# Kernel optimization log

Hardware: AMD Instinct MI355X
Metric: run time of the kernel (lower is better)

## Reference

```python
import jax, jax.numpy as jnp
import numpy as np

N_FEATURES = 170
D_MODEL = 64
N_HEADS = 4
ALPHA = 0.1
LN_EPS = 1e-5
LEAKY_SLOPE = 0.01  # torch F.leaky_relu default
N = 3 * N_FEATURES  # 510
B = 32


def setup_inputs() -> dict:
    key = jax.random.key(0)
    ks = jax.random.split(key, 10)
    D, H = D_MODEL, N_HEADS
    s = 1.0 / np.sqrt(D)
    return {
        "x": jax.random.normal(ks[0], (B, N, D), dtype=jnp.float32),
        "causal_graph": jax.random.uniform(ks[1], (N, N), dtype=jnp.float32),
        # nn.Linear(d_model, d_model*n_heads, bias=False): stored here as (D, H*D) for x @ W
        "W": jax.random.uniform(ks[2], (D, H * D), jnp.float32, -s, s),
        "attention_w": jax.random.normal(ks[3], (H, 2 * D), dtype=jnp.float32),
        # Conv2d(2, n_heads, 3, padding=1): OIHW kernel
        "conv_w": jax.random.uniform(ks[4], (H, 2, 3, 3), jnp.float32, -1/np.sqrt(18), 1/np.sqrt(18)),
        "conv_b": jax.random.uniform(ks[5], (H,), jnp.float32, -1/np.sqrt(18), 1/np.sqrt(18)),
        # nn.Linear(d_model, 2*d_model): stored as (D, 2D)
        "fcg_w": jax.random.uniform(ks[6], (D, 2 * D), jnp.float32, -s, s),
        "fcg_b": jax.random.uniform(ks[7], (2 * D,), jnp.float32, -s, s),
        "ln_g": jnp.ones((D,), jnp.float32),
        "ln_b": jnp.zeros((D,), jnp.float32),
    }


def reference(x, causal_graph, W, attention_w, conv_w, conv_b, fcg_w, fcg_b, ln_g, ln_b):
    Bz, Nn, D = x.shape
    H = N_HEADS
    # shared projection: (B, N, H, D)
    xt = (x @ W).reshape(Bz, Nn, H, D)
    # GAT-style additive scores: concat-dot decomposed into two dot products
    w1, w2 = attention_w[:, :D], attention_w[:, D:]  # each (H, D)
    s_i = jnp.einsum('bnhd,hd->bhn', xt, w1)  # source term
    s_j = jnp.einsum('bnhd,hd->bhn', xt, w2)  # target term
    e = s_i[:, :, :, None] + s_j[:, :, None, :]  # (B, H, N, N)
    A_eva = jnp.where(e >= 0, e, LEAKY_SLOPE * e)  # leaky_relu
    # fuse mean attention with causal graph via 3x3 conv
    A_mean = A_eva.mean(axis=1)  # (B, N, N)
    causal = jnp.broadcast_to(causal_graph[None], (Bz, Nn, Nn))
    stacked = jnp.stack([A_mean, causal], axis=1)  # (B, 2, N, N)
    A_st = jax.lax.conv_general_dilated(
        stacked, conv_w, window_strides=(1, 1), padding=((1, 1), (1, 1)),
        dimension_numbers=('NCHW', 'OIHW', 'NCHW'))
    A_st = A_st + conv_b[None, :, None, None]  # (B, H, N, N)
    A = jax.nn.softmax(ALPHA * A_eva + (1.0 - ALPHA) * A_st, axis=-1)
    # multi-head aggregation then head-mean
    out = jnp.einsum('bhnm,bmhd->bnhd', A, xt).mean(axis=2)  # (B, N, D)
    # GLU
    g = out @ fcg_w + fcg_b  # (B, N, 2D)
    a, b = g[..., :D], g[..., D:]
    glu = a * jax.nn.sigmoid(b)
    # residual + layernorm
    y = glu + x
    mu = y.mean(axis=-1, keepdims=True)
    var = ((y - mu) ** 2).mean(axis=-1, keepdims=True)
    y = (y - mu) * jax.lax.rsqrt(var + LN_EPS) * ln_g + ln_b
    return y, A
```

## Files before the change

### kernel.cpp

```cpp
#include <hip/hip_runtime.h>

#define Bz 32
#define Nn 510
#define Dd 64
#define Hh 4
#define HD_ 256
#define Kpad 512
#define ALPHA_ 0.1f
#define LNEPS 1e-5f
#define SLOPE 0.01f
#define NEG_INF -3.0e38f

typedef __attribute__((ext_vector_type(8))) short short8;
typedef __attribute__((ext_vector_type(4))) float floatx4;

__device__ inline float wredsum(float v) {
  #pragma unroll
  for (int off = 32; off; off >>= 1) v += __shfl_xor(v, off, 64);
  return v;
}
__device__ inline float wredmax(float v) {
  #pragma unroll
  for (int off = 32; off; off >>= 1) v = fmaxf(v, __shfl_xor(v, off, 64));
  return v;
}
__device__ inline unsigned short f2bf(float f) {
  unsigned int u = __float_as_uint(f);
  unsigned int r = (u + 0x7fffu + ((u >> 16) & 1u)) >> 16;
  return (unsigned short)r;
}

__global__ __launch_bounds__(256) void k1_xt(const float* __restrict__ x,
                                             const float* __restrict__ W,
                                             const float* __restrict__ attw,
                                             unsigned short* __restrict__ xtT,
                                             float* __restrict__ si,
                                             float* __restrict__ sj) {
  __shared__ float Wl[64][132];
  __shared__ float xr[32][68];
  const int t = threadIdx.x;
  const int rt = blockIdx.x;
  const int b = blockIdx.y;
  const int ch = blockIdx.z;
  #pragma unroll
  for (int k = 0; k < 8; k++) {
    int f = t + k * 256;
    int kr = f >> 5;
    int c = (f & 31) * 4;
    float4 v = *(const float4*)&W[kr * HD_ + ch * 128 + c];
    *(float4*)&Wl[kr][c] = v;
  }
  #pragma unroll
  for (int k = 0; k < 2; k++) {
    int f = t + k * 256;
    int r = f >> 4;
    int c = (f & 15) * 4;
    int row = rt * 32 + r;
    float4 v = make_float4(0.f, 0.f, 0.f, 0.f);
    if (row < Nn) v = *(const float4*)&x[(b * Nn + row) * Dd + c];
    *(float4*)&xr[r][c] = v;
  }
  __syncthreads();
  const int tr = t >> 5, tc = t & 31;
  const int rb = tr * 4, c0 = tc * 4;
  float acc[4][4] = {};
  #pragma unroll
  for (int k4 = 0; k4 < 16; k4++) {
    float4 xv[4];
    #pragma unroll
    for (int r = 0; r < 4; r++) xv[r] = *(float4*)&xr[rb + r][k4 * 4];
    #pragma unroll
    for (int kk = 0; kk < 4; kk++) {
      float4 wv = *(float4*)&Wl[k4 * 4 + kk][c0];
      #pragma unroll
      for (int r = 0; r < 4; r++) {
        float xs = (&xv[r].x)[kk];
        acc[r][0] = fmaf(xs, wv.x, acc[r][0]);
        acc[r][1] = fmaf(xs, wv.y, acc[r][1]);
        acc[r][2] = fmaf(xs, wv.z, acc[r][2]);
        acc[r][3] = fmaf(xs, wv.w, acc[r][3]);
      }
    }
  }
  const int colbase = ch * 128 + c0;
  const int h = colbase >> 6;
  const int dd = colbase & 63;
  const int m0r = rt * 32 + rb;
  #pragma unroll
  for (int cc = 0; cc < 4; cc++) {
    unsigned short* p = &xtT[((size_t)(b * 4 + h) * 64 + (dd + cc)) * Kpad + m0r];
    if (m0r + 3 < Nn) {
      ushort4 u;
      u.x = f2bf(acc[0][cc]); u.y = f2bf(acc[1][cc]);
      u.z = f2bf(acc[2][cc]); u.w = f2bf(acc[3][cc]);
      *(ushort4*)p = u;
    } else {
      #pragma unroll
      for (int r = 0; r < 4; r++) if (m0r + r < Nn) p[r] = f2bf(acc[r][cc]);
    }
  }
  float w1v[4], w2v[4];
  #pragma unroll
  for (int cc = 0; cc < 4; cc++) {
    w1v[cc] = attw[h * 128 + dd + cc];
    w2v[cc] = attw[h * 128 + 64 + dd + cc];
  }
  #pragma unroll
  for (int r = 0; r < 4; r++) {
    float p1 = acc[r][0] * w1v[0] + acc[r][1] * w1v[1] +
               acc[r][2] * w1v[2] + acc[r][3] * w1v[3];
    float p2 = acc[r][0] * w2v[0] + acc[r][1] * w2v[1] +
               acc[r][2] * w2v[2] + acc[r][3] * w2v[3];
    #pragma unroll
    for (int off = 1; off <= 8; off <<= 1) {
      p1 += __shfl_xor(p1, off, 64);
      p2 += __shfl_xor(p2, off, 64);
    }
    if ((tc & 15) == 0) {
      int row = m0r + r;
      if (row < Nn) {
        si[(b * 4 + h) * Nn + row] = p1;
        sj[(b * 4 + h) * Nn + row] = p2;
      }
    }
  }
}

__global__ __launch_bounds__(256) void k2_attn(const float* __restrict__ si,
                                               const float* __restrict__ sj,
                                               const float* __restrict__ causal,
                                               const float* __restrict__ convw,
                                               const float* __restrict__ convb,
                                               float* __restrict__ A) {
  __shared__ float am_t[10 * 8 * 68];
  __shared__ float cz_t[10 * 8 * 68];
  __shared__ float sjl[4 * 8 * 68];
  __shared__ float sil[4][12];
  const int t = threadIdx.x;
  const int i0 = blockIdx.x * 8;
  const int b = blockIdx.y;
  if (t < 40) {
    int h = t / 10, r = t % 10;
    int iq = i0 + r - 1;
    sil[h][r] = (iq >= 0 && iq < Nn) ? si[(b * 4 + h) * Nn + iq] : 0.f;
  }
  if (t >= 64 && t < 224) {
    int q = t - 64;
    int r = q >> 4, rem = q & 15;
    int e = rem >> 1, side = rem & 1;
    int idx = (r * 8 + e) * 68 + side * 65;
    am_t[idx] = 0.f;
    cz_t[idx] = 0.f;
  }
  for (int f = t; f < 2048; f += 256) {
    int h = f >> 9, j = f & 511;
    float v = (j < Nn) ? sj[(b * 4 + h) * Nn + j] : 0.f;
    sjl[(h * 8 + (j & 7)) * 68 + (j >> 3) + 1] = v;
  }
  __syncthreads();
  for (int f = t; f < 5120; f += 256) {
    int r = f >> 9, j = f & 511;
    int iq = i0 + r - 1;
    float am = 0.f, cz = 0.f;
    if (iq >= 0 && iq < Nn && j < Nn) {
      float s = 0.f;
      #pragma unroll
      for (int h = 0; h < 4; h++) {
        float e2 = sil[h][r] + sjl[(h * 8 + (j & 7)) * 68 + (j >> 3) + 1];
        s += (e2 >= 0.f) ? e2 : SLOPE * e2;
      }
      am = 0.25f * s;
      cz = causal[iq * Nn + j];
    }
    int idx = (r * 8 + (j & 7)) * 68 + (j >> 3) + 1;
    am_t[idx] = am;
    cz_t[idx] = cz;
  }
  __syncthreads();
  const int w = t >> 6, L = t & 63;
  const int j0 = L * 8;
  for (int pp = w; pp < 32; pp += 4) {
    const int il = pp >> 2, h = pp & 3;
    const int i = i0 + il;
    if (i >= Nn) continue;
    const int bh = b * 4 + h;
    const float sih = sil[h][il + 1];
    float cw[18];
    #pragma unroll
    for (int q = 0; q < 18; q++) cw[q] = convw[h * 18 + q];
    const float cb = convb[h];
    float conv[8];
    #pragma unroll
    for (int e = 0; e < 8; e++) conv[e] = cb;
    #pragma unroll
    for (int r3 = 0; r3 < 3; r3++) {
      const float* ba = &am_t[((il + r3) * 8) * 68];
      const float* bc = &cz_t[((il + r3) * 8) * 68];
      float a[10], c[10];
      a[0] = ba[7 * 68 + L];
      c[0] = bc[7 * 68 + L];
      #pragma unroll
      for (int e = 0; e < 8; e++) {
        a[1 + e] = ba[e * 68 + L + 1];
        c[1 + e] = bc[e * 68 + L + 1];
      }
      a[9] = ba[0 * 68 + L + 2];
      c[9] = bc[0 * 68 + L + 2];
      float w0 = cw[r3 * 3], w1 = cw[r3 * 3 + 1], w2 = cw[r3 * 3 + 2];
      float u0 = cw[9 + r3 * 3], u1 = cw[9 + r3 * 3 + 1], u2 = cw[9 + r3 * 3 + 2];
      #pragma unroll
      for (int e = 0; e < 8; e++) {
        float cv = conv[e];
        cv = fmaf(w0, a[e], cv);
        cv = fmaf(w1, a[e + 1], cv);
        cv = fmaf(w2, a[e + 2], cv);
        cv = fmaf(u0, c[e], cv);
        cv = fmaf(u1, c[e + 1], cv);
        cv = fmaf(u2, c[e + 2], cv);
        conv[e] = cv;
      }
    }
    float v[8];
    float mx = NEG_INF;
    #pragma unroll
    for (int e = 0; e < 8; e++) {
      float ee = sih + sjl[(h * 8 + e) * 68 + L + 1];
      float l = (ee >= 0.f) ? ee : SLOPE * ee;
      float val = ALPHA_ * l + (1.0f - ALPHA_) * conv[e];
      v[e] = (j0 + e < Nn) ? val : NEG_INF;
      mx = fmaxf(mx, v[e]);
    }
    mx = wredmax(mx);
    float p[8], s = 0.f;
    #pragma unroll
    for (int e = 0; e < 8; e++) {
      p[e] = __expf(v[e] - mx);
      s += p[e];
    }
    s = wredsum(s);
    const float inv = 1.f / s;
    #pragma unroll
    for (int e = 0; e < 8; e++) p[e] *= inv;
    float* Ar = &A[((size_t)bh * Nn + i) * Nn + j0];
    *(float4*)&Ar[0] = make_float4(p[0], p[1], p[2], p[3]);
    if (L < 63) {
      *(float4*)&Ar[4] = make_float4(p[4], p[5], p[6], p[7]);
    } else {
      *(float2*)&Ar[4] = make_float2(p[4], p[5]);
    }
  }
}

__global__ __launch_bounds__(256) void k3_out(const float* __restrict__ A,
                                              const unsigned short* __restrict__ xtT,
                                              const float* __restrict__ x,
                                              const float* __restrict__ fcgw,
                                              const float* __restrict__ fcgb,
                                              const float* __restrict__ lng,
                                              const float* __restrict__ lnb,
                                              float* __restrict__ y) {
  __shared__ unsigned short Asub[16 * 72];
  __shared__ unsigned short Xsub[64 * 72];
  __shared__ float ol[16][64];
  __shared__ float gl[2][128];
  const int t = threadIdx.x;
  const int n0 = blockIdx.x * 16;
  const int b = blockIdx.y;
  const int w = t >> 6, lane = t & 63;
  const int quad = lane >> 4, l16 = lane & 15;
  const int wc = w * 16;
  const int ar = t >> 4;
  const int amc = (t & 15) * 4;
  const int xd = t >> 2;
  const int xmc = (t & 3) * 16;
  floatx4 acc = {0.f, 0.f, 0.f, 0.f};
  for (int h = 0; h < 4; h++) {
    const float* Ab = &A[((size_t)(b * 4 + h) * Nn + n0) * Nn];
    const unsigned short* Xb = &xtT[(size_t)(b * 4 + h) * 64 * Kpad];
    for (int kt = 0; kt < 8; kt++) {
      const int m0 = kt * 64;
      __syncthreads();
      {
        int n = n0 + ar;
        int m = m0 + amc;
        float av[4] = {0.f, 0.f, 0.f, 0.f};
        if (n < Nn) {
          const float* src = &Ab[(size_t)ar * Nn + m];
          if (m + 3 < Nn) {
            *(float4*)av = *(const float4*)src;
          } else {
            int lim = Nn - m;
            #pragma unroll
            for (int q = 0; q < 4; q++) if (q < lim) av[q] = src[q];
          }
        }
        ushort4 u;
        u.x = f2bf(av[0]); u.y = f2bf(av[1]);
        u.z = f2bf(av[2]); u.w = f2bf(av[3]);
        *(ushort4*)&Asub[ar * 72 + amc] = u;
        const unsigned short* xs = &Xb[(size_t)xd * Kpad + m0 + xmc];
        short8 x0 = *(const short8*)&xs[0];
        short8 x1 = *(const short8*)&xs[8];
        *(short8*)&Xsub[xd * 72 + xmc] = x0;
        *(short8*)&Xsub[xd * 72 + xmc + 8] = x1;
      }
      __syncthreads();
      #pragma unroll
      for (int ks = 0; ks < 2; ks++) {
        short8 af = *(short8*)&Asub[l16 * 72 + ks * 32 + quad * 8];
        short8 bf = *(short8*)&Xsub[(wc + l16) * 72 + ks * 32 + quad * 8];
        acc = __builtin_amdgcn_mfma_f32_16x16x32_bf16(af, bf, acc, 0, 0, 0);
      }
    }
  }
  __syncthreads();
  #pragma unroll
  for (int reg = 0; reg < 4; reg++) {
    ol[quad * 4 + reg][wc + l16] = 0.25f * acc[reg];
  }
  __syncthreads();
  const int kk = t & 127;
  const int rg = t >> 7;
  for (int it = 0; it < 8; it++) {
    const int r = it * 2 + rg;
    const int row = n0 + r;
    float g = fcgb[kk];
    #pragma unroll
    for (int d = 0; d < 64; d++) g = fmaf(ol[r][d], fcgw[d * 128 + kk], g);
    gl[rg][kk] = g;
    __syncthreads();
    if (kk < 64 && row < Nn) {
      float a = gl[rg][kk];
      float bb = gl[rg][kk + 64];
      float glu = a / (1.f + __expf(-bb));
      float yv = glu + x[(b * Nn + row) * Dd + kk];
      float mu = wredsum(yv) * (1.f / 64.f);
      float dv = yv - mu;
      float var = wredsum(dv * dv) * (1.f / 64.f);
      float o = dv * rsqrtf(var + LNEPS) * lng[kk] + lnb[kk];
      y[(b * Nn + row) * Dd + kk] = o;
    }
    __syncthreads();
  }
}

extern "C" void kernel_launch(void* const* d_in, const int* in_sizes, int n_in,
                              void* d_out, int out_size, void* d_ws, size_t ws_size,
                              hipStream_t stream) {
  const float* x      = (const float*)d_in[0];
  const float* causal = (const float*)d_in[1];
  const float* W      = (const float*)d_in[2];
  const float* attw   = (const float*)d_in[3];
  const float* convw  = (const float*)d_in[4];
  const float* convb  = (const float*)d_in[5];
  const float* fcgw   = (const float*)d_in[6];
  const float* fcgb   = (const float*)d_in[7];
  const float* lng    = (const float*)d_in[8];
  const float* lnb    = (const float*)d_in[9];

  float* ws = (float*)d_ws;
  float* si = ws;
  float* sj = si + (size_t)Bz * Hh * Nn;
  unsigned short* xtT = (unsigned short*)(sj + (size_t)Bz * Hh * Nn + 16);
  size_t xtT_bytes = (size_t)Bz * Hh * Dd * Kpad * sizeof(unsigned short);

  float* yout = (float*)d_out;
  float* Aout = yout + (size_t)Bz * Nn * Dd;

  hipMemsetAsync(xtT, 0, xtT_bytes, stream);
  k1_xt <<<dim3(16, Bz, 2), 256, 0, stream>>>(x, W, attw, xtT, si, sj);
  k2_attn<<<dim3(64, Bz), 256, 0, stream>>>(si, sj, causal, convw, convb, Aout);
  k3_out <<<dim3(32, Bz), 256, 0, stream>>>(Aout, xtT, x, fcgw, fcgb, lng, lnb, yout);
}
```

Before: 308.5 us.

## Fuse softmax attention with aggregation/GLU and precompute batch-invariant causal conv

```diff
diff --git a/kernel.cpp b/kernel.cpp
--- a/kernel.cpp
+++ b/kernel.cpp
@@ -28,6 +28,9 @@
   unsigned int u = __float_as_uint(f);
   unsigned int r = (u + 0x7fffu + ((u >> 16) & 1u)) >> 16;
   return (unsigned short)r;
+}
+__device__ inline float bf2f(unsigned short u) {
+  return __uint_as_float(((unsigned int)u) << 16);
 }
 
 __global__ __launch_bounds__(256) void k1_xt(const float* __restrict__ x,
@@ -126,21 +129,65 @@
   }
 }
 
-__global__ __launch_bounds__(256) void k2_attn(const float* __restrict__ si,
-                                               const float* __restrict__ sj,
-                                               const float* __restrict__ causal,
-                                               const float* __restrict__ convw,
-                                               const float* __restrict__ convb,
-                                               float* __restrict__ A) {
-  __shared__ float am_t[10 * 8 * 68];
-  __shared__ float cz_t[10 * 8 * 68];
-  __shared__ float sjl[4 * 8 * 68];
-  __shared__ float sil[4][12];
+__global__ __launch_bounds__(256) void k2a(const float* __restrict__ causal,
+                                           const float* __restrict__ convw,
+                                           const float* __restrict__ convb,
+                                           float* __restrict__ cc) {
+  __shared__ float clds[3][520];
+  const int t = threadIdx.x;
+  const int i = blockIdx.x;
+  for (int f = t; f < 3 * 514; f += 256) {
+    int r = f / 514, jj = f - r * 514;
+    int iq = i - 1 + r, j = jj - 1;
+    clds[r][jj] = (iq >= 0 && iq < Nn && j >= 0 && j < Nn) ? causal[iq * Nn + j] : 0.f;
+  }
+  __syncthreads();
+  const int j0 = t * 2;
+  #pragma unroll
+  for (int h = 0; h < 4; h++) {
+    float u[9];
+    #pragma unroll
+    for (int q = 0; q < 9; q++) u[q] = convw[h * 18 + 9 + q];
+    float s0 = convb[h], s1 = convb[h];
+    #pragma unroll
+    for (int r3 = 0; r3 < 3; r3++) {
+      #pragma unroll
+      for (int dj = 0; dj < 3; dj++) {
+        float wv = u[r3 * 3 + dj];
+        s0 = fmaf(wv, clds[r3][j0 + dj], s0);
+        s1 = fmaf(wv, clds[r3][j0 + 1 + dj], s1);
+      }
+    }
+    float* o = &cc[((size_t)h * Nn + i) * 512 + j0];
+    o[0] = 0.9f * s0;
+    o[1] = 0.9f * s1;
+  }
+}
+
+__global__ __launch_bounds__(256) void k23(const float* __restrict__ si,
+                                           const float* __restrict__ sj,
+                                           const float* __restrict__ cc,
+                                           const unsigned short* __restrict__ xtT,
+                                           const float* __restrict__ convw,
+                                           const float* __restrict__ x,
+                                           const float* __restrict__ fcgw,
+                                           const float* __restrict__ fcgb,
+                                           const float* __restrict__ lng,
+                                           const float* __restrict__ lnb,
+                                           float* __restrict__ A,
+                                           float* __restrict__ y) {
+  __shared__ unsigned short am_t[10 * 8 * 66];
+  __shared__ unsigned short sjl[4 * 8 * 66];
+  __shared__ unsigned short Al[9 * 520];
+  __shared__ float ol[8][64];
+  __shared__ float gl[2][128];
+  __shared__ float sil[4][10];
   const int t = threadIdx.x;
   const int i0 = blockIdx.x * 8;
   const int b = blockIdx.y;
+  if (t < 130) ((uint2*)&Al[8 * 520])[t] = make_uint2(0u, 0u);
   if (t < 40) {
-    int h = t / 10, r = t % 10;
+    int h = t / 10, r = t - h * 10;
     int iq = i0 + r - 1;
     sil[h][r] = (iq >= 0 && iq < Nn) ? si[(b * 4 + h) * Nn + iq] : 0.f;
   }
@@ -148,182 +195,117 @@
     int q = t - 64;
     int r = q >> 4, rem = q & 15;
     int e = rem >> 1, side = rem & 1;
-    int idx = (r * 8 + e) * 68 + side * 65;
-    am_t[idx] = 0.f;
-    cz_t[idx] = 0.f;
+    am_t[(r * 8 + e) * 66 + side * 65] = 0;
   }
   for (int f = t; f < 2048; f += 256) {
     int h = f >> 9, j = f & 511;
     float v = (j < Nn) ? sj[(b * 4 + h) * Nn + j] : 0.f;
-    sjl[(h * 8 + (j & 7)) * 68 + (j >> 3) + 1] = v;
+    sjl[(h * 8 + (j & 7)) * 66 + (j >> 3) + 1] = f2bf(v);
   }
   __syncthreads();
   for (int f = t; f < 5120; f += 256) {
     int r = f >> 9, j = f & 511;
     int iq = i0 + r - 1;
-    float am = 0.f, cz = 0.f;
+    float am = 0.f;
     if (iq >= 0 && iq < Nn && j < Nn) {
       float s = 0.f;
       #pragma unroll
       for (int h = 0; h < 4; h++) {
-        float e2 = sil[h][r] + sjl[(h * 8 + (j & 7)) * 68 + (j >> 3) + 1];
+        float e2 = sil[h][r] + bf2f(sjl[(h * 8 + (j & 7)) * 66 + (j >> 3) + 1]);
         s += (e2 >= 0.f) ? e2 : SLOPE * e2;
       }
       am = 0.25f * s;
-      cz = causal[iq * Nn + j];
-    }
-    int idx = (r * 8 + (j & 7)) * 68 + (j >> 3) + 1;
-    am_t[idx] = am;
-    cz_t[idx] = cz;
+    }
+    am_t[(r * 8 + (j & 7)) * 66 + (j >> 3) + 1] = f2bf(am);
   }
   __syncthreads();
   const int w = t >> 6, L = t & 63;
+  const int quad = L >> 4, l16 = L & 15;
   const int j0 = L * 8;
-  for (int pp = w; pp < 32; pp += 4) {
-    const int il = pp >> 2, h = pp & 3;
-    const int i = i0 + il;
-    if (i >= Nn) continue;
-    const int bh = b * 4 + h;
-    const float sih = sil[h][il + 1];
-    float cw[18];
-    #pragma unroll
-    for (int q = 0; q < 18; q++) cw[q] = convw[h * 18 + q];
-    const float cb = convb[h];
-    float conv[8];
-    #pragma unroll
-    for (int e = 0; e < 8; e++) conv[e] = cb;
-    #pragma unroll
-    for (int r3 = 0; r3 < 3; r3++) {
-      const float* ba = &am_t[((il + r3) * 8) * 68];
-      const float* bc = &cz_t[((il + r3) * 8) * 68];
-      float a[10], c[10];
-      a[0] = ba[7 * 68 + L];
-      c[0] = bc[7 * 68 + L];
-      #pragma unroll
-      for (int e = 0; e < 8; e++) {
-        a[1 + e] = ba[e * 68 + L + 1];
-        c[1 + e] = bc[e * 68 + L + 1];
-      }
-      a[9] = ba[0 * 68 + L + 2];
-      c[9] = bc[0 * 68 + L + 2];
-      float w0 = cw[r3 * 3], w1 = cw[r3 * 3 + 1], w2 = cw[r3 * 3 + 2];
-      float u0 = cw[9 + r3 * 3], u1 = cw[9 + r3 * 3 + 1], u2 = cw[9 + r3 * 3 + 2];
-      #pragma unroll
-      for (int e = 0; e < 8; e++) {
-        float cv = conv[e];
-        cv = fmaf(w0, a[e], cv);
-        cv = fmaf(w1, a[e + 1], cv);
-        cv = fmaf(w2, a[e + 2], cv);
-        cv = fmaf(u0, c[e], cv);
-        cv = fmaf(u1, c[e + 1], cv);
-        cv = fmaf(u2, c[e + 2], cv);
-        conv[e] = cv;
-      }
-    }
-    float v[8];
-    float mx = NEG_INF;
-    #pragma unroll
-    for (int e = 0; e < 8; e++) {
-      float ee = sih + sjl[(h * 8 + e) * 68 + L + 1];
-      float l = (ee >= 0.f) ? ee : SLOPE * ee;
-      float val = ALPHA_ * l + (1.0f - ALPHA_) * conv[e];
-      v[e] = (j0 + e < Nn) ? val : NEG_INF;
-      mx = fmaxf(mx, v[e]);
-    }
-    mx = wredmax(mx);
-    float p[8], s = 0.f;
-    #pragma unroll
-    for (int e = 0; e < 8; e++) {
-      p[e] = __expf(v[e] - mx);
-      s += p[e];
-    }
-    s = wredsum(s);
-    const float inv = 1.f / s;
-    #pragma unroll
-    for (int e = 0; e < 8; e++) p[e] *= inv;
-    float* Ar = &A[((size_t)bh * Nn + i) * Nn + j0];
-    *(float4*)&Ar[0] = make_float4(p[0], p[1], p[2], p[3]);
-    if (L < 63) {
-      *(float4*)&Ar[4] = make_float4(p[4], p[5], p[6], p[7]);
-    } else {
-      *(float2*)&Ar[4] = make_float2(p[4], p[5]);
-    }
-  }
-}
-
-__global__ __launch_bounds__(256) void k3_out(const float* __restrict__ A,
-                                              const unsigned short* __restrict__ xtT,
-                                              const float* __restrict__ x,
-                                              const float* __restrict__ fcgw,
-                                              const float* __restrict__ fcgb,
-                                              const float* __restrict__ lng,
-                                              const float* __restrict__ lnb,
-                                              float* __restrict__ y) {
-  __shared__ unsigned short Asub[16 * 72];
-  __shared__ unsigned short Xsub[64 * 72];
-  __shared__ float ol[16][64];
-  __shared__ float gl[2][128];
-  const int t = threadIdx.x;
-  const int n0 = blockIdx.x * 16;
-  const int b = blockIdx.y;
-  const int w = t >> 6, lane = t & 63;
-  const int quad = lane >> 4, l16 = lane & 15;
-  const int wc = w * 16;
-  const int ar = t >> 4;
-  const int amc = (t & 15) * 4;
-  const int xd = t >> 2;
-  const int xmc = (t & 3) * 16;
   floatx4 acc = {0.f, 0.f, 0.f, 0.f};
   for (int h = 0; h < 4; h++) {
-    const float* Ab = &A[((size_t)(b * 4 + h) * Nn + n0) * Nn];
-    const unsigned short* Xb = &xtT[(size_t)(b * 4 + h) * 64 * Kpad];
-    for (int kt = 0; kt < 8; kt++) {
-      const int m0 = kt * 64;
-      __syncthreads();
-      {
-        int n = n0 + ar;
-        int m = m0 + amc;
-        float av[4] = {0.f, 0.f, 0.f, 0.f};
-        if (n < Nn) {
-          const float* src = &Ab[(size_t)ar * Nn + m];
-          if (m + 3 < Nn) {
-            *(float4*)av = *(const float4*)src;
-          } else {
-            int lim = Nn - m;
-            #pragma unroll
-            for (int q = 0; q < 4; q++) if (q < lim) av[q] = src[q];
-          }
+    float cw9[9];
+    #pragma unroll
+    for (int q = 0; q < 9; q++) cw9[q] = convw[h * 18 + q];
+    #pragma unroll
+    for (int rr = 0; rr < 2; rr++) {
+      const int il = w * 2 + rr;
+      const int i = i0 + il;
+      if (i < Nn) {
+        float conv[8];
+        #pragma unroll
+        for (int e = 0; e < 8; e++) conv[e] = 0.f;
+        #pragma unroll
+        for (int r3 = 0; r3 < 3; r3++) {
+          const unsigned short* ba = &am_t[((il + r3) * 8) * 66];
+          float a[10];
+          a[0] = bf2f(ba[7 * 66 + L]);
+          #pragma unroll
+          for (int e = 0; e < 8; e++) a[1 + e] = bf2f(ba[e * 66 + L + 1]);
+          a[9] = bf2f(ba[0 * 66 + L + 2]);
+          float w0 = cw9[r3 * 3], w1 = cw9[r3 * 3 + 1], w2 = cw9[r3 * 3 + 2];
+          #pragma unroll
+          for (int e = 0; e < 8; e++)
+            conv[e] = fmaf(w0, a[e], fmaf(w1, a[e + 1], fmaf(w2, a[e + 2], conv[e])));
         }
-        ushort4 u;
-        u.x = f2bf(av[0]); u.y = f2bf(av[1]);
-        u.z = f2bf(av[2]); u.w = f2bf(av[3]);
-        *(ushort4*)&Asub[ar * 72 + amc] = u;
-        const unsigned short* xs = &Xb[(size_t)xd * Kpad + m0 + xmc];
-        short8 x0 = *(const short8*)&xs[0];
-        short8 x1 = *(const short8*)&xs[8];
-        *(short8*)&Xsub[xd * 72 + xmc] = x0;
-        *(short8*)&Xsub[xd * 72 + xmc + 8] = x1;
-      }
-      __syncthreads();
-      #pragma unroll
-      for (int ks = 0; ks < 2; ks++) {
-        short8 af = *(short8*)&Asub[l16 * 72 + ks * 32 + quad * 8];
-        short8 bf = *(short8*)&Xsub[(wc + l16) * 72 + ks * 32 + quad * 8];
-        acc = __builtin_amdgcn_mfma_f32_16x16x32_bf16(af, bf, acc, 0, 0, 0);
-      }
-    }
-  }
-  __syncthreads();
+        float ccv[8];
+        const float* ccp = &cc[((size_t)h * Nn + i) * 512 + j0];
+        *(float4*)&ccv[0] = *(const float4*)&ccp[0];
+        *(float4*)&ccv[4] = *(const float4*)&ccp[4];
+        const float sih = sil[h][il + 1];
+        float v[8];
+        float mx = NEG_INF;
+        #pragma unroll
+        for (int e = 0; e < 8; e++) {
+          float e2 = sih + bf2f(sjl[(h * 8 + e) * 66 + L + 1]);
+          float l = (e2 >= 0.f) ? e2 : SLOPE * e2;
+          float val = fmaf(0.9f, conv[e], fmaf(ALPHA_, l, ccv[e]));
+          v[e] = (j0 + e < Nn) ? val : NEG_INF;
+          mx = fmaxf(mx, v[e]);
+        }
+        mx = wredmax(mx);
+        float p[8], s = 0.f;
+        #pragma unroll
+        for (int e = 0; e < 8; e++) {
+          p[e] = __expf(v[e] - mx);
+          s += p[e];
+        }
+        s = wredsum(s);
+        const float inv = 1.f / s;
+        #pragma unroll
+        for (int e = 0; e < 8; e++) p[e] *= inv;
+        float* Ar = &A[((size_t)(b * 4 + h) * Nn + i) * Nn + j0];
+        *(float4*)&Ar[0] = make_float4(p[0], p[1], p[2], p[3]);
+        if (L < 63) *(float4*)&Ar[4] = make_float4(p[4], p[5], p[6], p[7]);
+        else        *(float2*)&Ar[4] = make_float2(p[4], p[5]);
+        short8 ps;
+        #pragma unroll
+        for (int e = 0; e < 8; e++) ps[e] = (short)f2bf(p[e]);
+        *(short8*)&Al[il * 520 + j0] = ps;
+      }
+    }
+    __syncthreads();
+    const unsigned short* Xb = xtT + ((size_t)(b * 4 + h) * 64 + (w * 16 + l16)) * Kpad;
+    const unsigned short* Ap = &Al[(l16 < 8 ? l16 : 8) * 520 + quad * 8];
+    #pragma unroll 4
+    for (int ks = 0; ks < 16; ks++) {
+      short8 af = *(const short8*)&Ap[ks * 32];
+      short8 bf = *(const short8*)&Xb[ks * 32 + quad * 8];
+      acc = __builtin_amdgcn_mfma_f32_16x16x32_bf16(af, bf, acc, 0, 0, 0);
+    }
+    __syncthreads();
+  }
   #pragma unroll
   for (int reg = 0; reg < 4; reg++) {
-    ol[quad * 4 + reg][wc + l16] = 0.25f * acc[reg];
+    int row = quad * 4 + reg;
+    if (row < 8) ol[row][w * 16 + l16] = 0.25f * acc[reg];
   }
   __syncthreads();
   const int kk = t & 127;
   const int rg = t >> 7;
-  for (int it = 0; it < 8; it++) {
+  for (int it = 0; it < 4; it++) {
     const int r = it * 2 + rg;
-    const int row = n0 + r;
+    const int row = i0 + r;
     float g = fcgb[kk];
     #pragma unroll
     for (int d = 0; d < 64; d++) g = fmaf(ol[r][d], fcgw[d * 128 + kk], g);
@@ -362,13 +344,15 @@
   float* si = ws;
   float* sj = si + (size_t)Bz * Hh * Nn;
   unsigned short* xtT = (unsigned short*)(sj + (size_t)Bz * Hh * Nn + 16);
-  size_t xtT_bytes = (size_t)Bz * Hh * Dd * Kpad * sizeof(unsigned short);
+  size_t xtT_elems = (size_t)Bz * Hh * Dd * Kpad;
+  float* cc = (float*)(xtT + xtT_elems);
 
   float* yout = (float*)d_out;
   float* Aout = yout + (size_t)Bz * Nn * Dd;
 
-  hipMemsetAsync(xtT, 0, xtT_bytes, stream);
-  k1_xt <<<dim3(16, Bz, 2), 256, 0, stream>>>(x, W, attw, xtT, si, sj);
-  k2_attn<<<dim3(64, Bz), 256, 0, stream>>>(si, sj, causal, convw, convb, Aout);
-  k3_out <<<dim3(32, Bz), 256, 0, stream>>>(Aout, xtT, x, fcgw, fcgb, lng, lnb, yout);
-}
+  hipMemsetAsync(xtT, 0, xtT_elems * sizeof(unsigned short), stream);
+  k1_xt<<<dim3(16, Bz, 2), 256, 0, stream>>>(x, W, attw, xtT, si, sj);
+  k2a  <<<Nn, 256, 0, stream>>>(causal, convw, convb, cc);
+  k23  <<<dim3(64, Bz), 256, 0, stream>>>(si, sj, cc, xtT, convw, x,
+                                          fcgw, fcgb, lng, lnb, Aout, yout);
+}
```

Result: no change. 308.8 us (+0.1%).
